# Performance work log

Hardware: AMD Instinct MI355X
Metric: run time of the kernel (lower is better)

## Reference

```python
import jax, jax.numpy as jnp
import numpy as np

N = 1_000_000
DATA_DIM = 16
N_COND = 8            # conditions 1..8; condition 0 uses the base model (id 0)
N_BUCKETS = 8         # uniform time intervals per condition on [0,1)
N_MODELS = N_COND * N_BUCKETS + 1   # 65, matches num_models+1 in the torch ctor
HIDDEN = 6            # SimpleModel(data_dim, hidden=6, time_embed_dim=6)
IN_DIM = DATA_DIM + 1 # MLP input is cat([data, t], dim=1)


def setup_inputs() -> dict:
    key = jax.random.key(0)
    k_data, k_cond, k_t, k_w1, k_b1, k_w2, k_b2 = jax.random.split(key, 7)
    data = jax.random.normal(k_data, (N, DATA_DIM), dtype=jnp.float32)
    cond = jax.random.randint(k_cond, (N, 1), 0, N_COND + 1).astype(jnp.float32)  # 0..8
    t = jax.random.uniform(k_t, (N, 1), dtype=jnp.float32)                        # [0,1)
    x = jnp.concatenate([data, cond, t], axis=1)  # [N, DATA_DIM+2]
    s1 = 1.0 / np.sqrt(IN_DIM)
    s2 = 1.0 / np.sqrt(HIDDEN)
    W1 = jax.random.uniform(k_w1, (N_MODELS, IN_DIM, HIDDEN), jnp.float32, -s1, s1)
    b1 = jax.random.uniform(k_b1, (N_MODELS, HIDDEN), jnp.float32, -s1, s1)
    W2 = jax.random.uniform(k_w2, (N_MODELS, HIDDEN, DATA_DIM), jnp.float32, -s2, s2)
    b2 = jax.random.uniform(k_b2, (N_MODELS, DATA_DIM), jnp.float32, -s2, s2)
    return {"x": x, "W1": W1, "b1": b1, "W2": W2, "b2": b2}


def _route(cond_f, t):
    # Bucket routing: cond 0 -> model 0 on [0,1); cond c>=1 -> models 1 + (c-1)*8 + floor(t*8).
    # Equivalent to the torch per-(c, [t1,t2)) masked dispatch with uniform breakpoints.
    c = cond_f.astype(jnp.int32)
    bucket = jnp.clip(jnp.floor(t * N_BUCKETS).astype(jnp.int32), 0, N_BUCKETS - 1)
    return jnp.where(c == 0, 0, 1 + (c - 1) * N_BUCKETS + bucket)


def reference(x, W1, b1, W2, b2):
    data = x[:, :-2]
    cond = x[:, -2]
    t = x[:, -1]
    mid = _route(cond, t)                                   # [N] expert id per row
    xin = jnp.concatenate([data, t[:, None]], axis=1)       # [N, IN_DIM]
    # Fused gather-MLP: gather each row's tiny expert weights and apply the 2-layer MLP.
    h = jax.nn.relu(jnp.einsum('ni,nih->nh', xin, W1[mid]) + b1[mid])   # [N, HIDDEN]
    out = jnp.einsum('nh,nhd->nd', h, W2[mid]) + b2[mid]                # [N, DATA_DIM]
    return out
```

## Files before the change

kernel.cpp:

```cpp
#include <hip/hip_runtime.h>


#define NMODELS 65
#define WPM 220
#define BLOCK 1024

__global__ __launch_bounds__(BLOCK) void mvf_kernel(
    const float* __restrict__ x,
    const float* __restrict__ W1,
    const float* __restrict__ b1,
    const float* __restrict__ W2,
    const float* __restrict__ b2,
    float* __restrict__ out,
    int npts)
{
    __shared__ float wlds[WPM][NMODELS];
    const int tid = threadIdx.x;

    for (int e = tid; e < NMODELS * WPM; e += BLOCK) {
        const int m = e / WPM, k = e % WPM;
        float v;
        if (k < 102)      v = W1[m * 102 + k];
        else if (k < 108) v = b1[m * 6 + (k - 102)];
        else if (k < 204) v = W2[m * 96 + (k - 108)];
        else              v = b2[m * 16 + (k - 204)];
        wlds[k][m] = v;
    }
    __syncthreads();

    const int p = blockIdx.x * BLOCK + tid;
    if (p >= npts) return;

    float xf[18];
    const float2* xr = (const float2*)(x + (long)p * 18);
    #pragma unroll
    for (int i = 0; i < 9; ++i) {
        float2 v = xr[i];
        xf[2 * i] = v.x;
        xf[2 * i + 1] = v.y;
    }
    const float t = xf[17];
    const int c = (int)xf[16];
    int bucket = (int)floorf(t * 8.0f);
    bucket = bucket < 0 ? 0 : (bucket > 7 ? 7 : bucket);
    const int mid = (c == 0) ? 0 : 1 + (c - 1) * 8 + bucket;

    xf[16] = t;

    float h[6];
    #pragma unroll
    for (int j = 0; j < 6; ++j) h[j] = wlds[102 + j][mid];
    #pragma unroll
    for (int i = 0; i < 17; ++i) {
        const float xi = xf[i];
        #pragma unroll
        for (int j = 0; j < 6; ++j)
            h[j] = fmaf(xi, wlds[i * 6 + j][mid], h[j]);
    }
    #pragma unroll
    for (int j = 0; j < 6; ++j) h[j] = h[j] > 0.0f ? h[j] : 0.0f;

    float o[16];
    #pragma unroll
    for (int d = 0; d < 16; ++d) o[d] = wlds[204 + d][mid];
    #pragma unroll
    for (int j = 0; j < 6; ++j) {
        const float hj = h[j];
        #pragma unroll
        for (int d = 0; d < 16; ++d)
            o[d] = fmaf(hj, wlds[108 + j * 16 + d][mid], o[d]);
    }

    float4* orow = (float4*)(out + (long)p * 16);
    #pragma unroll
    for (int q = 0; q < 4; ++q) {
        orow[q] = make_float4(o[4 * q], o[4 * q + 1], o[4 * q + 2], o[4 * q + 3]);
    }
}

extern "C" void kernel_launch(void* const* d_in, const int* in_sizes, int n_in,
                              void* d_out, int out_size, void* d_ws, size_t ws_size,
                              hipStream_t stream) {
    const float* x  = (const float*)d_in[0];
    const float* W1 = (const float*)d_in[1];
    const float* b1 = (const float*)d_in[2];
    const float* W2 = (const float*)d_in[3];
    const float* b2 = (const float*)d_in[4];
    float* out = (float*)d_out;

    const int npts = in_sizes[0] / 18;
    const int grid = (npts + BLOCK - 1) / BLOCK;
    mvf_kernel<<<grid, BLOCK, 0, stream>>>(x, W1, b1, W2, b2, out, npts);
}
```

Measured before the change: 49.76 us.

## Pack expert weights as float4 in LDS and process two rows per thread

Stores the shared-memory weight table as float4 chunks interleaved per model, so each thread fetches four weights with one LDS read instead of four scalar reads. Each thread now handles two consecutive rows, loading them as nine float4 reads, and the block size is halved with a 4-blocks-per-CU launch bound. This cuts LDS instruction count and the number of blocks that must each reload the full weight table. It raises register pressure from the two-row state. It also assumes an even row count, since the second row is processed without a bounds check.

Measured after the change: 48.90 us. About the same (-1.7%).

```diff
diff --git a/kernel.cpp b/kernel.cpp
--- a/kernel.cpp
+++ b/kernel.cpp
@@ -3,9 +3,10 @@
 
 #define NMODELS 65
 #define WPM 220
-#define BLOCK 1024
+#define NCHUNK 55
+#define BLOCK 512
 
-__global__ __launch_bounds__(BLOCK) void mvf_kernel(
+__global__ __launch_bounds__(BLOCK, 4) void mvf_kernel(
     const float* __restrict__ x,
     const float* __restrict__ W1,
     const float* __restrict__ b1,
@@ -14,9 +15,10 @@
     float* __restrict__ out,
     int npts)
 {
-    __shared__ float wlds[WPM][NMODELS];
+    __shared__ float4 wlds[NCHUNK][NMODELS];
     const int tid = threadIdx.x;
 
+    float* wf = (float*)wlds;
     for (int e = tid; e < NMODELS * WPM; e += BLOCK) {
         const int m = e / WPM, k = e % WPM;
         float v;
@@ -24,58 +26,116 @@
         else if (k < 108) v = b1[m * 6 + (k - 102)];
         else if (k < 204) v = W2[m * 96 + (k - 108)];
         else              v = b2[m * 16 + (k - 204)];
-        wlds[k][m] = v;
+        wf[(k >> 2) * (NMODELS * 4) + m * 4 + (k & 3)] = v;
     }
     __syncthreads();
 
-    const int p = blockIdx.x * BLOCK + tid;
-    if (p >= npts) return;
+    const int q = blockIdx.x * BLOCK + tid;
+    const int p0 = 2 * q;
+    if (p0 >= npts) return;
 
-    float xf[18];
-    const float2* xr = (const float2*)(x + (long)p * 18);
+    float xf[36];
+    {
+        const float4* xr4 = (const float4*)(x + (long)p0 * 18);
+        #pragma unroll
+        for (int i = 0; i < 9; ++i) {
+            float4 v = xr4[i];
+            xf[4 * i + 0] = v.x;
+            xf[4 * i + 1] = v.y;
+            xf[4 * i + 2] = v.z;
+            xf[4 * i + 3] = v.w;
+        }
+    }
+    #define XF(pt, i) xf[(pt) * 18 + (i)]
+
+    int mid[2];
+    float tt[2];
     #pragma unroll
-    for (int i = 0; i < 9; ++i) {
-        float2 v = xr[i];
-        xf[2 * i] = v.x;
-        xf[2 * i + 1] = v.y;
+    for (int pt = 0; pt < 2; ++pt) {
+        const float t = XF(pt, 17);
+        const int c = (int)XF(pt, 16);
+        int bucket = (int)floorf(t * 8.0f);
+        bucket = bucket < 0 ? 0 : (bucket > 7 ? 7 : bucket);
+        mid[pt] = (c == 0) ? 0 : 1 + (c - 1) * 8 + bucket;
+        tt[pt] = t;
     }
-    const float t = xf[17];
-    const int c = (int)xf[16];
-    int bucket = (int)floorf(t * 8.0f);
-    bucket = bucket < 0 ? 0 : (bucket > 7 ? 7 : bucket);
-    const int mid = (c == 0) ? 0 : 1 + (c - 1) * 8 + bucket;
 
-    xf[16] = t;
+    #define CH(cc, pt) wlds[cc][mid[pt]]
 
-    float h[6];
+    float h[2][6];
     #pragma unroll
-    for (int j = 0; j < 6; ++j) h[j] = wlds[102 + j][mid];
+    for (int pt = 0; pt < 2; ++pt) {
+        float4 c24 = CH(24, pt);
+        float4 c25 = CH(25, pt);
+        float4 c26 = CH(26, pt);
+        const float t = tt[pt];
+        h[pt][0] = fmaf(t, c24.x, c25.z);
+        h[pt][1] = fmaf(t, c24.y, c25.w);
+        h[pt][2] = fmaf(t, c24.z, c26.x);
+        h[pt][3] = fmaf(t, c24.w, c26.y);
+        h[pt][4] = fmaf(t, c25.x, c26.z);
+        h[pt][5] = fmaf(t, c25.y, c26.w);
+    }
     #pragma unroll
-    for (int i = 0; i < 17; ++i) {
-        const float xi = xf[i];
+    for (int r = 0; r < 8; ++r) {
+        #pragma unroll
+        for (int pt = 0; pt < 2; ++pt) {
+            float4 a = CH(3 * r + 0, pt);
+            float4 b = CH(3 * r + 1, pt);
+            float4 d = CH(3 * r + 2, pt);
+            const float x0 = XF(pt, 2 * r), x1 = XF(pt, 2 * r + 1);
+            h[pt][0] = fmaf(x0, a.x, h[pt][0]);
+            h[pt][1] = fmaf(x0, a.y, h[pt][1]);
+            h[pt][2] = fmaf(x0, a.z, h[pt][2]);
+            h[pt][3] = fmaf(x0, a.w, h[pt][3]);
+            h[pt][4] = fmaf(x0, b.x, h[pt][4]);
+            h[pt][5] = fmaf(x0, b.y, h[pt][5]);
+            h[pt][0] = fmaf(x1, b.z, h[pt][0]);
+            h[pt][1] = fmaf(x1, b.w, h[pt][1]);
+            h[pt][2] = fmaf(x1, d.x, h[pt][2]);
+            h[pt][3] = fmaf(x1, d.y, h[pt][3]);
+            h[pt][4] = fmaf(x1, d.z, h[pt][4]);
+            h[pt][5] = fmaf(x1, d.w, h[pt][5]);
+        }
+    }
+    #pragma unroll
+    for (int pt = 0; pt < 2; ++pt)
         #pragma unroll
         for (int j = 0; j < 6; ++j)
-            h[j] = fmaf(xi, wlds[i * 6 + j][mid], h[j]);
+            h[pt][j] = h[pt][j] > 0.0f ? h[pt][j] : 0.0f;
+
+    #pragma unroll
+    for (int half = 0; half < 2; ++half) {
+        #pragma unroll
+        for (int pt = 0; pt < 2; ++pt) {
+            float o[8];
+            {
+                float4 ba = CH(51 + 2 * half, pt);
+                float4 bb = CH(52 + 2 * half, pt);
+                o[0] = ba.x; o[1] = ba.y; o[2] = ba.z; o[3] = ba.w;
+                o[4] = bb.x; o[5] = bb.y; o[6] = bb.z; o[7] = bb.w;
+            }
+            #pragma unroll
+            for (int j = 0; j < 6; ++j) {
+                float4 A = CH(27 + 4 * j + 2 * half + 0, pt);
+                float4 B = CH(27 + 4 * j + 2 * half + 1, pt);
+                const float hj = h[pt][j];
+                o[0] = fmaf(hj, A.x, o[0]);
+                o[1] = fmaf(hj, A.y, o[1]);
+                o[2] = fmaf(hj, A.z, o[2]);
+                o[3] = fmaf(hj, A.w, o[3]);
+                o[4] = fmaf(hj, B.x, o[4]);
+                o[5] = fmaf(hj, B.y, o[5]);
+                o[6] = fmaf(hj, B.z, o[6]);
+                o[7] = fmaf(hj, B.w, o[7]);
+            }
+            float4* orow = (float4*)(out + (long)(p0 + pt) * 16 + half * 8);
+            orow[0] = make_float4(o[0], o[1], o[2], o[3]);
+            orow[1] = make_float4(o[4], o[5], o[6], o[7]);
+        }
     }
-    #pragma unroll
-    for (int j = 0; j < 6; ++j) h[j] = h[j] > 0.0f ? h[j] : 0.0f;
-
-    float o[16];
-    #pragma unroll
-    for (int d = 0; d < 16; ++d) o[d] = wlds[204 + d][mid];
-    #pragma unroll
-    for (int j = 0; j < 6; ++j) {
-        const float hj = h[j];
-        #pragma unroll
-        for (int d = 0; d < 16; ++d)
-            o[d] = fmaf(hj, wlds[108 + j * 16 + d][mid], o[d]);
-    }
-
-    float4* orow = (float4*)(out + (long)p * 16);
-    #pragma unroll
-    for (int q = 0; q < 4; ++q) {
-        orow[q] = make_float4(o[4 * q], o[4 * q + 1], o[4 * q + 2], o[4 * q + 3]);
-    }
+    #undef CH
+    #undef XF
 }
 
 extern "C" void kernel_launch(void* const* d_in, const int* in_sizes, int n_in,
@@ -89,6 +149,7 @@
     float* out = (float*)d_out;
 
     const int npts = in_sizes[0] / 18;
-    const int grid = (npts + BLOCK - 1) / BLOCK;
+    const int npairs = (npts + 1) / 2;
+    const int grid = (npairs + BLOCK - 1) / BLOCK;
     mvf_kernel<<<grid, BLOCK, 0, stream>>>(x, W1, b1, W2, b2, out, npts);
 }
```

## Sort rows by expert in LDS and use packed bf16 dot2 for MLP

Applied to the files above, without the earlier changes.

Weights are converted to bf16 pairs and laid out as uint4 chunks per model, so the MLP runs with v_dot2_f32_bf16 and 128-bit LDS reads. Each block also counting-sorts its rows by expert id through LDS histograms, so neighbouring lanes read the same weights and LDS bank conflicts drop. Inputs and hidden activations are rounded to bf16, which lowers accuracy. The sort adds several barriers and atomics per block.

Measured after the change: 56.85 us (median of 2 runs). 1.14x slower.

```diff
diff --git a/kernel.cpp b/kernel.cpp
--- a/kernel.cpp
+++ b/kernel.cpp
@@ -2,10 +2,26 @@
 
 
 #define NMODELS 65
-#define WPM 220
+#define NCHUNK 30
 #define BLOCK 1024
 
-__global__ __launch_bounds__(BLOCK) void mvf_kernel(
+__device__ inline unsigned f2bf(float f) {
+    unsigned u = __builtin_bit_cast(unsigned, f);
+    u += 0x7fffu + ((u >> 16) & 1u);
+    return u >> 16;
+}
+__device__ inline float dot2bf(unsigned a, unsigned b, float c) {
+    float r;
+    asm("v_dot2_f32_bf16 %0, %1, %2, %3" : "=v"(r) : "v"(a), "v"(b), "v"(c));
+    return r;
+}
+__device__ inline unsigned cvtpk(float lo, float hi) {
+    unsigned r;
+    asm("v_cvt_pk_bf16_f32 %0, %1, %2" : "=v"(r) : "v"(lo), "v"(hi));
+    return r;
+}
+
+__global__ __launch_bounds__(BLOCK, 4) void mvf_kernel(
     const float* __restrict__ x,
     const float* __restrict__ W1,
     const float* __restrict__ b1,
@@ -14,68 +30,146 @@
     float* __restrict__ out,
     int npts)
 {
-    __shared__ float wlds[WPM][NMODELS];
+    __shared__ unsigned wlds[NCHUNK * NMODELS * 4];
+    __shared__ unsigned xlds[9 * BLOCK];
+    __shared__ unsigned bidx[BLOCK];
+    __shared__ int hist[NMODELS];
+    __shared__ int base_[NMODELS];
+
     const int tid = threadIdx.x;
+    if (tid < NMODELS) hist[tid] = 0;
 
-    for (int e = tid; e < NMODELS * WPM; e += BLOCK) {
-        const int m = e / WPM, k = e % WPM;
-        float v;
-        if (k < 102)      v = W1[m * 102 + k];
-        else if (k < 108) v = b1[m * 6 + (k - 102)];
-        else if (k < 204) v = W2[m * 96 + (k - 108)];
-        else              v = b2[m * 16 + (k - 204)];
-        wlds[k][m] = v;
+    const long pbase = (long)blockIdx.x * BLOCK;
+    const int nvalid = min(BLOCK, npts - (int)pbase);
+    const bool valid = tid < nvalid;
+
+    float xf[18];
+    if (valid) {
+        const float2* xr = (const float2*)(x + (pbase + tid) * 18);
+        #pragma unroll
+        for (int i = 0; i < 9; ++i) {
+            float2 v = xr[i];
+            xf[2 * i] = v.x; xf[2 * i + 1] = v.y;
+        }
+    } else {
+        #pragma unroll
+        for (int i = 0; i < 18; ++i) xf[i] = 0.0f;
+    }
+
+    for (int e = tid; e < NMODELS * NCHUNK * 4; e += BLOCK) {
+        const int m = e / (NCHUNK * 4);
+        const int r = e - m * (NCHUNK * 4);
+        const int c = r >> 2, s = r & 3;
+        float flo, fhi;
+        if (c < 12) {
+            const int j = c >> 1;
+            const int q = (c & 1) * 4 + s;
+            flo = W1[m * 102 + (2 * q) * 6 + j];
+            fhi = W1[m * 102 + (2 * q + 1) * 6 + j];
+        } else if (c == 12) {
+            flo = W1[m * 102 + 96 + s];
+            fhi = b1[m * 6 + s];
+        } else if (c == 13) {
+            if (s < 2) { flo = W1[m * 102 + 96 + 4 + s]; fhi = b1[m * 6 + 4 + s]; }
+            else       { flo = 0.0f; fhi = 0.0f; }
+        } else {
+            const int d = c - 14;
+            if (s < 3) {
+                flo = W2[m * 96 + (2 * s) * 16 + d];
+                fhi = W2[m * 96 + (2 * s + 1) * 16 + d];
+            } else {
+                flo = b2[m * 16 + d];
+                fhi = 0.0f;
+            }
+        }
+        wlds[c * (NMODELS * 4) + m * 4 + s] = f2bf(flo) | (f2bf(fhi) << 16);
     }
     __syncthreads();
 
-    const int p = blockIdx.x * BLOCK + tid;
-    if (p >= npts) return;
+    int mid = 0, myoff = 0;
+    if (valid) {
+        const float t = xf[17];
+        const int c = (int)xf[16];
+        int bucket = (int)floorf(t * 8.0f);
+        bucket = bucket < 0 ? 0 : (bucket > 7 ? 7 : bucket);
+        mid = (c == 0) ? 0 : 1 + (c - 1) * 8 + bucket;
+        myoff = atomicAdd(&hist[mid], 1);
+        #pragma unroll
+        for (int k = 0; k < 8; ++k)
+            xlds[k * BLOCK + tid] = cvtpk(xf[2 * k], xf[2 * k + 1]);
+        xlds[8 * BLOCK + tid] = cvtpk(t, 1.0f);
+    }
+    __syncthreads();
 
-    float xf[18];
-    const float2* xr = (const float2*)(x + (long)p * 18);
+    if (tid == 0) {
+        int acc = 0;
+        for (int m = 0; m < NMODELS; ++m) { base_[m] = acc; acc += hist[m]; }
+    }
+    __syncthreads();
+
+    if (valid) bidx[base_[mid] + myoff] = ((unsigned)mid << 16) | (unsigned)tid;
+    __syncthreads();
+
+    if (!valid) return;
+
+    const unsigned en = bidx[tid];
+    const int src = (int)(en & 0xffffu);
+    const int pm  = (int)(en >> 16);
+
+    unsigned xp[9];
     #pragma unroll
-    for (int i = 0; i < 9; ++i) {
-        float2 v = xr[i];
-        xf[2 * i] = v.x;
-        xf[2 * i + 1] = v.y;
-    }
-    const float t = xf[17];
-    const int c = (int)xf[16];
-    int bucket = (int)floorf(t * 8.0f);
-    bucket = bucket < 0 ? 0 : (bucket > 7 ? 7 : bucket);
-    const int mid = (c == 0) ? 0 : 1 + (c - 1) * 8 + bucket;
+    for (int k = 0; k < 9; ++k) xp[k] = xlds[k * BLOCK + src];
 
-    xf[16] = t;
+    const uint4* wl4 = (const uint4*)wlds;
+    #define CH(cc) wl4[(cc) * NMODELS + pm]
 
     float h[6];
-    #pragma unroll
-    for (int j = 0; j < 6; ++j) h[j] = wlds[102 + j][mid];
-    #pragma unroll
-    for (int i = 0; i < 17; ++i) {
-        const float xi = xf[i];
-        #pragma unroll
-        for (int j = 0; j < 6; ++j)
-            h[j] = fmaf(xi, wlds[i * 6 + j][mid], h[j]);
+    {
+        uint4 cA = CH(12), cB = CH(13);
+        h[0] = dot2bf(xp[8], cA.x, 0.0f);
+        h[1] = dot2bf(xp[8], cA.y, 0.0f);
+        h[2] = dot2bf(xp[8], cA.z, 0.0f);
+        h[3] = dot2bf(xp[8], cA.w, 0.0f);
+        h[4] = dot2bf(xp[8], cB.x, 0.0f);
+        h[5] = dot2bf(xp[8], cB.y, 0.0f);
     }
     #pragma unroll
-    for (int j = 0; j < 6; ++j) h[j] = h[j] > 0.0f ? h[j] : 0.0f;
+    for (int j = 0; j < 6; ++j) {
+        uint4 A = CH(2 * j);
+        uint4 B = CH(2 * j + 1);
+        float a = h[j];
+        a = dot2bf(xp[0], A.x, a);
+        a = dot2bf(xp[1], A.y, a);
+        a = dot2bf(xp[2], A.z, a);
+        a = dot2bf(xp[3], A.w, a);
+        a = dot2bf(xp[4], B.x, a);
+        a = dot2bf(xp[5], B.y, a);
+        a = dot2bf(xp[6], B.z, a);
+        a = dot2bf(xp[7], B.w, a);
+        h[j] = a > 0.0f ? a : 0.0f;
+    }
+
+    unsigned hp0 = cvtpk(h[0], h[1]);
+    unsigned hp1 = cvtpk(h[2], h[3]);
+    unsigned hp2 = cvtpk(h[4], h[5]);
+    const unsigned hp3 = 0x00003F80u;
 
     float o[16];
     #pragma unroll
-    for (int d = 0; d < 16; ++d) o[d] = wlds[204 + d][mid];
+    for (int d = 0; d < 16; ++d) {
+        uint4 W = CH(14 + d);
+        float a = dot2bf(hp0, W.x, 0.0f);
+        a = dot2bf(hp1, W.y, a);
+        a = dot2bf(hp2, W.z, a);
+        a = dot2bf(hp3, W.w, a);
+        o[d] = a;
+    }
+    #undef CH
+
+    float4* orow = (float4*)(out + (pbase + src) * 16);
     #pragma unroll
-    for (int j = 0; j < 6; ++j) {
-        const float hj = h[j];
-        #pragma unroll
-        for (int d = 0; d < 16; ++d)
-            o[d] = fmaf(hj, wlds[108 + j * 16 + d][mid], o[d]);
-    }
-
-    float4* orow = (float4*)(out + (long)p * 16);
-    #pragma unroll
-    for (int q = 0; q < 4; ++q) {
-        orow[q] = make_float4(o[4 * q], o[4 * q + 1], o[4 * q + 2], o[4 * q + 3]);
-    }
+    for (int g = 0; g < 4; ++g)
+        orow[g] = make_float4(o[4 * g], o[4 * g + 1], o[4 * g + 2], o[4 * g + 3]);
 }
 
 extern "C" void kernel_launch(void* const* d_in, const int* in_sizes, int n_in,
```
